# Kernel optimization log

Measured on AMD Instinct MI355X. Metric: run time of the kernel, lower is better.

Reference implementation:

```python
import jax, jax.numpy as jnp
import numpy as np

NUM_HEADS = 8
HEAD_SPLITS = [2, 3, 3]   # heads per conv window group (windows 3,5,7)


def _dwconv(x, w, b):
    # depthwise conv2d, SAME padding; x [B,Cg,H,W], w [Cg,1,k,k]
    k = w.shape[-1]
    pad = k // 2
    out = jax.lax.conv_general_dilated(
        x, w, window_strides=(1, 1), padding=[(pad, pad), (pad, pad)],
        feature_group_count=x.shape[1])
    return out + b[None, :, None, None]


def setup_inputs() -> dict:
    key = jax.random.key(0)
    ks = jax.random.split(key, 8)
    B, Hs, Ws, C = 16, 56, 56, 512
    N = 1 + Hs * Ws
    Ch = C // NUM_HEADS
    inp = {
        "x": jax.random.normal(ks[0], (B, N, C), dtype=jnp.float32),
        "qkv_w": jax.random.normal(ks[1], (3 * C, C), dtype=jnp.float32) * 0.02,
        "qkv_b": jnp.zeros((3 * C,), dtype=jnp.float32),
        "proj_w": jax.random.normal(ks[2], (C, C), dtype=jnp.float32) * 0.02,
        "proj_b": jnp.zeros((C,), dtype=jnp.float32),
        "conv_w3": jax.random.normal(ks[3], (2 * Ch, 1, 3, 3), dtype=jnp.float32) * 0.1,
        "conv_b3": jnp.zeros((2 * Ch,), dtype=jnp.float32),
        "conv_w5": jax.random.normal(ks[4], (3 * Ch, 1, 5, 5), dtype=jnp.float32) * 0.1,
        "conv_b5": jnp.zeros((3 * Ch,), dtype=jnp.float32),
        "conv_w7": jax.random.normal(ks[5], (3 * Ch, 1, 7, 7), dtype=jnp.float32) * 0.1,
        "conv_b7": jnp.zeros((3 * Ch,), dtype=jnp.float32),
        "H": 56,
        "W": 56,
    }
    return inp


def reference(x, qkv_w, qkv_b, proj_w, proj_b,
              conv_w3, conv_b3, conv_w5, conv_b5, conv_w7, conv_b7, H, W):
    B, N, C = x.shape
    h = NUM_HEADS
    Ch = C // h
    scale = Ch ** -0.5

    # qkv projection -> [3, B, h, N, Ch]
    qkv = (x @ qkv_w.T + qkv_b).reshape(B, N, 3, h, Ch)
    qkv = jnp.transpose(qkv, (2, 0, 3, 1, 4))
    q, k, v = qkv[0], qkv[1], qkv[2]

    # linear-attention factorization: softmax over tokens, then small Ch x Ch matmuls
    k_sm = jax.nn.softmax(k, axis=2)                     # softmax over N
    kv = jnp.einsum('bhnk,bhnd->bhkd', k_sm, v)          # [B,h,Ch,Ch]
    factor_att = jnp.einsum('bhnk,bhkd->bhnd', q, kv)    # [B,h,N,Ch]

    # conv relative-position encoding (CoaT ConvRelPosEnc)
    q_img = q[:, :, 1:, :]                               # drop CLS token
    v_img = v[:, :, 1:, :]
    v_img = jnp.transpose(v_img, (0, 1, 3, 2)).reshape(B, h * Ch, H, W)
    splits = np.cumsum([s * Ch for s in HEAD_SPLITS])[:-1]
    p3, p5, p7 = jnp.split(v_img, splits, axis=1)
    conv_v = jnp.concatenate([
        _dwconv(p3, conv_w3, conv_b3),
        _dwconv(p5, conv_w5, conv_b5),
        _dwconv(p7, conv_w7, conv_b7)], axis=1)           # [B,h*Ch,H,W]
    conv_v = jnp.transpose(conv_v.reshape(B, h, Ch, H * W), (0, 1, 3, 2))
    ev = q_img * conv_v                                   # [B,h,HW,Ch]
    crpe = jnp.concatenate(
        [jnp.zeros((B, h, 1, Ch), dtype=x.dtype), ev], axis=2)

    out = scale * factor_att + crpe                       # [B,h,N,Ch]
    out = jnp.transpose(out, (0, 2, 1, 3)).reshape(B, N, C)
    return out @ proj_w.T + proj_b
```

## Files before the change

kernel.cpp:

```cpp
#include <hip/hip_runtime.h>
#include <stdint.h>

#define NHEADS 8
#define NTOK   3137
#define BATCH  16
#define CDIM   512
#define MT     (BATCH*NTOK)

typedef unsigned short u16;
typedef float f32x4  __attribute__((ext_vector_type(4)));
typedef short bf16x8 __attribute__((ext_vector_type(8)));

__device__ __forceinline__ float bf2f(u16 u){
  union { uint32_t i; float f; } x; x.i = ((uint32_t)u) << 16; return x.f;
}
__device__ __forceinline__ u16 f2bf(float f){
  union { float f; uint32_t i; } x; x.f = f;
  uint32_t r = x.i + 0x7fffu + ((x.i >> 16) & 1u);
  return (u16)(r >> 16);
}
__device__ __forceinline__ void async_ld16(void* lds, const void* g){
  __builtin_amdgcn_global_load_lds((const __attribute__((address_space(1))) void*)g,
                                   (__attribute__((address_space(3))) void*)lds, 16, 0, 0);
}
#define BARM()   asm volatile("s_barrier" ::: "memory")
#define WAITV(N) asm volatile("s_waitcnt vmcnt(" #N ")" ::: "memory")
#define MFMA16(d,a,b) d = __builtin_amdgcn_mfma_f32_16x16x32_bf16(a,b,d,0,0,0)

__global__ void cvt_all(const float* __restrict__ x, u16* __restrict__ x_bf,
                        const float* __restrict__ qw, u16* __restrict__ qw_bf,
                        const float* __restrict__ pw, u16* __restrict__ pw_bf){
  const int n4x = (MT*512)/4, n4q = (1536*512)/4, n4p = (512*512)/4;
  int i = blockIdx.x * blockDim.x + threadIdx.x;
  const float* src; u16* dst; int j = i;
  if (i < n4x){ src = x; dst = x_bf; }
  else if (i < n4x + n4q){ src = qw; dst = qw_bf; j = i - n4x; }
  else if (i < n4x + n4q + n4p){ src = pw; dst = pw_bf; j = i - n4x - n4q; }
  else return;
  float4 v = ((const float4*)src)[j];
  uint32_t lo = ((uint32_t)f2bf(v.y) << 16) | f2bf(v.x);
  uint32_t hi = ((uint32_t)f2bf(v.w) << 16) | f2bf(v.z);
  ((uint2*)dst)[j] = make_uint2(lo, hi);
}

template<int MODE>
__global__ __launch_bounds__(256) void gemmM(
    const u16* __restrict__ A, const u16* __restrict__ Bw, const float* __restrict__ bias,
    u16* __restrict__ q_s, u16* __restrict__ k_s, u16* __restrict__ v_s,
    float* __restrict__ outF, int M)
{
  __shared__ __align__(16) u16 smem[256*64];
  const int t = threadIdx.x;
  const int w = t >> 6, l = t & 63;
  const int wr = w >> 1, wc = w & 1;
  const int lr = l & 15, lg = l >> 4;

  const int nx = gridDim.x;
  const int nwg = nx * gridDim.y;
  const int orig = blockIdx.y * nx + blockIdx.x;
  const int q8 = nwg >> 3, r8 = nwg & 7;
  const int xcd = orig & 7;
  const int wgid = (xcd < r8 ? xcd*(q8+1) : r8*(q8+1) + (xcd-r8)*q8) + (orig >> 3);
  const int n0 = (wgid % nx) * 128;
  const int m0 = (wgid / nx) * 128;

  f32x4 acc[4][4];
#pragma unroll
  for (int i=0;i<4;i++)
#pragma unroll
    for (int j=0;j<4;j++) acc[i][j] = (f32x4){0.f,0.f,0.f,0.f};

  u16* da = smem;
  u16* db = smem + 128*64;

  for (int kt = 0; kt < 8; ++kt){
    const int k0 = kt*64;
#pragma unroll
    for (int j=0;j<4;j++){
      int qc = t + 256*j;
      int R = qc >> 3, c = qc & 7;
      int cs = (c ^ (R & 7)) * 8;
      int ar = m0 + R; if (ar > M-1) ar = M-1;
      async_ld16(&da[qc*8], &A[(size_t)ar*512 + k0 + cs]);
    }
#pragma unroll
    for (int j=0;j<4;j++){
      int qc = t + 256*j;
      int R = qc >> 3, c = qc & 7;
      int cs = (c ^ (R & 7)) * 8;
      async_ld16(&db[qc*8], &Bw[(size_t)(n0+R)*512 + k0 + cs]);
    }
    WAITV(0);
    BARM();
    __builtin_amdgcn_s_setprio(1);
#pragma unroll
    for (int ks=0; ks<2; ks++){
      bf16x8 af[4], bfv[4];
      int chunk = ks*4 + lg;
#pragma unroll
      for (int fi=0;fi<4;fi++){
        int row = wr*64 + fi*16 + lr;
        af[fi] = *(const bf16x8*)&da[row*64 + ((chunk ^ (row & 7))*8)];
      }
#pragma unroll
      for (int fj=0;fj<4;fj++){
        int col = wc*64 + fj*16 + lr;
        bfv[fj] = *(const bf16x8*)&db[col*64 + ((chunk ^ (col & 7))*8)];
      }
#pragma unroll
      for (int fi=0;fi<4;fi++)
#pragma unroll
        for (int fj=0;fj<4;fj++)
          acc[fi][fj] = __builtin_amdgcn_mfma_f32_16x16x32_bf16(af[fi], bfv[fj], acc[fi][fj], 0, 0, 0);
    }
    __builtin_amdgcn_s_setprio(0);
    BARM();
  }

  float bvv[4];
#pragma unroll
  for (int fj=0;fj<4;fj++) bvv[fj] = bias[n0 + wc*64 + fj*16 + lr];
  const int colo = n0 + wc*64;

  if (MODE == 0){
    u16* warea = smem + w * 4096;
#pragma unroll
    for (int fi=0;fi<4;fi++)
#pragma unroll
      for (int fj=0;fj<4;fj++)
#pragma unroll
        for (int r=0;r<4;r++)
          warea[(fi*16 + lg*4 + r)*64 + fj*16 + lr] = f2bf(acc[fi][fj][r] + bvv[fj]);
    const int part = colo >> 9;
    const int hq   = (colo >> 6) & 7;
    u16* dst = (part == 0) ? q_s : ((part == 1) ? k_s : v_s);
    const int rsub = l >> 3;
    const int csub = (l & 7) * 8;
#pragma unroll
    for (int pass=0; pass<8; ++pass){
      int rl = pass*8 + rsub;
      int m = m0 + wr*64 + rl;
      if (m < M){
        int bb = m / NTOK;
        int n  = m - bb*NTOK;
        uint4 vv = *(const uint4*)&warea[rl*64 + csub];
        *(uint4*)&dst[((size_t)(bb*8 + hq)*NTOK + n)*64 + csub] = vv;
      }
    }
  } else {
    float* warea = (float*)smem + w * 2048;
    const int rsub = l >> 4;
    const int csub = (l & 15) * 4;
#pragma unroll
    for (int p=0; p<2; ++p){
#pragma unroll
      for (int fh=0; fh<2; fh++){
        int fi = p*2 + fh;
#pragma unroll
        for (int fj=0;fj<4;fj++)
#pragma unroll
          for (int r=0;r<4;r++)
            warea[(fh*16 + lg*4 + r)*64 + fj*16 + lr] = acc[fi][fj][r] + bvv[fj];
      }
#pragma unroll
      for (int pass=0; pass<8; ++pass){
        int rl = pass*4 + rsub;
        int m = m0 + wr*64 + p*32 + rl;
        if (m < M){
          float4 vv = *(const float4*)&warea[rl*64 + csub];
          *(float4*)&outF[(size_t)m*512 + colo + csub] = vv;
        }
      }
    }
  }
}

__global__ __launch_bounds__(256) void kv_mfma(
    const u16* __restrict__ k_s, const u16* __restrict__ v_s,
    float* __restrict__ kv_p, float* __restrict__ s_p)
{
  __shared__ __align__(16) u16 ekT[64*64];
  __shared__ __align__(16) u16 vT[64*64];
  __shared__ float part_s[32*64];
  const int t  = threadIdx.x;
  const int bh = blockIdx.x;
  const int qq = blockIdx.y;
  const size_t base = (size_t)bh * NTOK * 64;
  const int c_beg = qq*6 + (qq < 2 ? qq : 2);
  const int c_end = c_beg + 6 + (qq < 2 ? 1 : 0);
  const int w = t >> 6, l = t & 63;
  const int lr = l & 15, lg = l >> 4;
  const int nl0 = t >> 3;
  const int dc  = (t & 7) * 8;

  f32x4 acc[4];
#pragma unroll
  for (int j=0;j<4;j++) acc[j] = (f32x4){0.f,0.f,0.f,0.f};
  float s_loc[8];
#pragma unroll
  for (int i=0;i<8;i++) s_loc[i] = 0.f;

  auto LD = [&](int ch, int half, uint4& kv, uint4& vv){
    int n = ch*64 + nl0 + half*32;
    if (n < NTOK){
      kv = *(const uint4*)&k_s[base + (size_t)n*64 + dc];
      vv = *(const uint4*)&v_s[base + (size_t)n*64 + dc];
    } else {
      kv = make_uint4(0u,0u,0u,0u);
      vv = make_uint4(0u,0u,0u,0u);
    }
  };

  uint4 kc0, vc0, kc1, vc1, kn0, vn0, kn1, vn1;
  LD(c_beg, 0, kc0, vc0);
  LD(c_beg, 1, kc1, vc1);

  for (int ch = c_beg; ch < c_end; ++ch){
    const int n0c = ch*64;
    if (ch + 1 < c_end){ LD(ch+1, 0, kn0, vn0); LD(ch+1, 1, kn1, vn1); }
    __syncthreads();
#pragma unroll
    for (int half=0; half<2; ++half){
      const uint4& kvec = half ? kc1 : kc0;
      const uint4& vvec = half ? vc1 : vc0;
      int nloc = nl0 + half*32;
      bool valid = (n0c + nloc < NTOK);
      const u16* kp = (const u16*)&kvec;
      const u16* vp = (const u16*)&vvec;
      const int nc = nloc >> 3, ne = nloc & 7;
#pragma unroll
      for (int i=0;i<8;i++){
        float e = valid ? __expf(bf2f(kp[i])) : 0.f;
        s_loc[i] += e;
        int row = dc + i;
        int pos = row*64 + ((nc ^ (row & 7) ^ ((row >> 3) & 7))*8) + ne;
        ekT[pos] = f2bf(e);
        vT[pos]  = vp[i];
      }
    }
    __syncthreads();
    __builtin_amdgcn_s_setprio(1);
#pragma unroll
    for (int ks=0; ks<2; ks++){
      int chnk = ks*4 + lg;
      int arow = w*16 + lr;
      bf16x8 af = *(const bf16x8*)&ekT[arow*64 + ((chnk ^ (arow & 7) ^ ((arow >> 3) & 7))*8)];
#pragma unroll
      for (int fj=0; fj<4; fj++){
        int col = fj*16 + lr;
        bf16x8 bv = *(const bf16x8*)&vT[col*64 + ((chnk ^ (col & 7) ^ ((col >> 3) & 7))*8)];
        MFMA16(acc[fj], af, bv);
      }
    }
    __builtin_amdgcn_s_setprio(0);
    kc0 = kn0; vc0 = vn0; kc1 = kn1; vc1 = vn1;
  }

  const size_t obase = ((size_t)qq*128 + bh) * 4096;
#pragma unroll
  for (int fj=0; fj<4; fj++)
#pragma unroll
    for (int r=0; r<4; r++)
      kv_p[obase + (size_t)(w*16 + lg*4 + r)*64 + fj*16 + lr] = acc[fj][r];

#pragma unroll
  for (int i=0;i<8;i++) part_s[nl0*64 + dc + i] = s_loc[i];
  __syncthreads();
  if (t < 64){
    float s = 0.f;
    for (int r=0;r<32;r++) s += part_s[r*64 + t];
    s_p[((size_t)qq*128 + bh)*64 + t] = s;
  }
}

__global__ void kv_reduce(const float* __restrict__ kv_p, const float* __restrict__ s_p,
                          const u16* __restrict__ q_s, u16* __restrict__ kvT,
                          u16* __restrict__ out_pre){
  __shared__ float red[64*64];
  const int bh = blockIdx.x, t = threadIdx.x;
  const int b = bh >> 3, h = bh & 7;
  const int k = t >> 2;
  const float q0 = bf2f(q_s[(size_t)bh*NTOK*64 + k]);
  float S = 0.f;
#pragma unroll
  for (int hf=0; hf<8; hf++) S += s_p[(hf*128 + bh)*64 + k];
  const float rS = 1.f / S;
  for (int i=0;i<16;i++){
    int e = t*16 + i;
    int d = (t & 3)*16 + i;
    float v = 0.f;
#pragma unroll
    for (int hf=0; hf<8; hf++) v += kv_p[(size_t)(hf*128 + bh)*4096 + e];
    float val = v * rS;
    kvT[(size_t)bh*4096 + d*64 + k] = f2bf(val);
    red[k*64 + d] = val * q0;
  }
  __syncthreads();
  if (t < 64){
    float s = 0.f;
    for (int r=0;r<64;r++) s += red[r*64 + t];
    out_pre[((size_t)b*NTOK)*CDIM + h*64 + t] = f2bf(0.125f * s);
  }
}

template<int R>
__global__ __launch_bounds__(256) void conv_fa(
    const u16* __restrict__ v_s, const u16* __restrict__ q_s,
    const u16* __restrict__ kvT,
    const float* __restrict__ wsrc, const float* __restrict__ bsrc,
    int h0, u16* __restrict__ out_pre)
{
  constexpr int KK = 2*R + 1;
  constexpr int TAPS = KK*KK;
  __shared__ __align__(16) u16 smem[8192 + KK*3584];
  u16* vt = smem + 8192;
  const int t = threadIdx.x;
  const int y  = blockIdx.x;
  const int hh = blockIdx.y;
  const int b  = blockIdx.z;
  const int h  = h0 + hh;
  const int bh = b*8 + h;
  const size_t base = (size_t)bh * NTOK * 64;
  const int n0 = 1 + y*56;

#pragma unroll
  for (int j=0;j<2;j++){
    int qq = t + 256*j;
    int row = qq >> 3, c = qq & 7;
    int cs = (c ^ (row & 7)) * 8;
    int n = n0 + row; if (n > NTOK-1) n = NTOK-1;
    async_ld16(&smem[qq*8], &q_s[base + (size_t)n*64 + cs]);
    async_ld16(&smem[4096 + qq*8], &kvT[(size_t)bh*4096 + row*64 + cs]);
  }
  for (int ry=0; ry<KK; ry++){
    int yy = y - R + ry;
    for (int idx = t; idx < 448; idx += 256){
      uint4 val = make_uint4(0u,0u,0u,0u);
      if (yy >= 0 && yy < 56)
        val = *(const uint4*)&v_s[base + (size_t)(1 + yy*56)*64 + idx*8];
      *(uint4*)&vt[ry*3584 + idx*8] = val;
    }
  }
  __syncthreads();

  const int w = t >> 6, l = t & 63;
  const int lr = l & 15, lg = l >> 4;
  f32x4 fac[4];
#pragma unroll
  for (int j=0;j<4;j++) fac[j] = (f32x4){0.f,0.f,0.f,0.f};
#pragma unroll
  for (int ks=0; ks<2; ks++){
    int chunk = ks*4 + lg;
    int arow = w*16 + lr;
    bf16x8 af = *(const bf16x8*)&smem[arow*64 + ((chunk ^ (arow & 7))*8)];
#pragma unroll
    for (int fj=0; fj<4; fj++){
      int col = fj*16 + lr;
      bf16x8 bvv = *(const bf16x8*)&smem[4096 + col*64 + ((chunk ^ (col & 7))*8)];
      MFMA16(fac[fj], af, bvv);
    }
  }

  const int d = l;
  const int xg = w;
  float wreg[TAPS];
#pragma unroll
  for (int i=0;i<TAPS;i++) wreg[i] = wsrc[(hh*64 + d)*TAPS + i];
  const float bias = bsrc[hh*64 + d];
  float creg[14];
#pragma unroll
  for (int i=0;i<14;i++) creg[i] = bias;
  const int x0 = xg * 14;
#pragma unroll
  for (int ry=0; ry<KK; ry++){
    float rw[14 + 2*R];
#pragma unroll
    for (int i=0; i<14+2*R; i++){
      int xx = x0 - R + i;
      rw[i] = (xx >= 0 && xx < 56) ? bf2f(vt[ry*3584 + xx*64 + d]) : 0.f;
    }
#pragma unroll
    for (int xi=0; xi<14; xi++)
#pragma unroll
      for (int rx=0; rx<KK; rx++)
        creg[xi] += rw[xi+rx] * wreg[ry*KK + rx];
  }

  float qv[14];
#pragma unroll
  for (int xi=0; xi<14; xi++){
    int row = x0 + xi;
    int chunk = d >> 3, e = d & 7;
    qv[xi] = bf2f(smem[row*64 + ((chunk ^ (row & 7))*8) + e]);
  }

  __syncthreads();
  float* fa = (float*)smem;
#pragma unroll
  for (int fj=0; fj<4; fj++)
#pragma unroll
    for (int r=0; r<4; r++)
      fa[(w*16 + lg*4 + r)*64 + fj*16 + lr] = 0.125f * fac[fj][r];
  __syncthreads();

#pragma unroll
  for (int xi=0; xi<14; xi++){
    int nn = n0 + x0 + xi;
    out_pre[((size_t)b*NTOK + nn)*CDIM + h*64 + d] =
        f2bf(fa[(x0 + xi)*64 + d] + creg[xi]*qv[xi]);
  }
}

extern "C" void kernel_launch(void* const* d_in, const int* in_sizes, int n_in,
                              void* d_out, int out_size, void* d_ws, size_t ws_size,
                              hipStream_t stream)
{
  const float* x      = (const float*)d_in[0];
  const float* qkv_w  = (const float*)d_in[1];
  const float* qkv_b  = (const float*)d_in[2];
  const float* proj_w = (const float*)d_in[3];
  const float* proj_b = (const float*)d_in[4];
  const float* w3 = (const float*)d_in[5];
  const float* b3 = (const float*)d_in[6];
  const float* w5 = (const float*)d_in[7];
  const float* b5 = (const float*)d_in[8];
  const float* w7 = (const float*)d_in[9];
  const float* b7 = (const float*)d_in[10];
  float* out = (float*)d_out;

  char* ws = (char*)d_ws;
  size_t off = 0;
  auto alloc = [&](size_t bytes) -> void* {
    void* p = ws + off;
    off += (bytes + 255) & ~(size_t)255;
    return p;
  };
  u16*   x_bf     = (u16*)alloc((size_t)MT*512*2);
  u16*   qkvw_bf  = (u16*)alloc((size_t)1536*512*2);
  u16*   projw_bf = (u16*)alloc((size_t)512*512*2);
  u16*   q_s      = (u16*)alloc((size_t)128*NTOK*64*2);
  u16*   k_s      = (u16*)alloc((size_t)128*NTOK*64*2);
  u16*   v_s      = (u16*)alloc((size_t)128*NTOK*64*2);
  u16*   kvT      = (u16*)alloc((size_t)128*4096*2);
  float* kv_p     = (float*)alloc((size_t)8*128*4096*4);
  float* s_p      = (float*)alloc((size_t)8*128*64*4);
  u16*   out_pre  = x_bf;

  { int n4 = (MT*512 + 1536*512 + 512*512)/4;
    cvt_all<<<(n4+255)/256, 256, 0, stream>>>(x, x_bf, qkv_w, qkvw_bf, proj_w, projw_bf); }

  gemmM<0><<<dim3(12, 393), 256, 0, stream>>>(x_bf, qkvw_bf, qkv_b, q_s, k_s, v_s, nullptr, MT);

  kv_mfma<<<dim3(128, 8), 256, 0, stream>>>(k_s, v_s, kv_p, s_p);
  kv_reduce<<<128, 256, 0, stream>>>(kv_p, s_p, q_s, kvT, out_pre);

  conv_fa<1><<<dim3(56, 2, 16), 256, 0, stream>>>(v_s, q_s, kvT, w3, b3, 0, out_pre);
  conv_fa<2><<<dim3(56, 3, 16), 256, 0, stream>>>(v_s, q_s, kvT, w5, b5, 2, out_pre);
  conv_fa<3><<<dim3(56, 3, 16), 256, 0, stream>>>(v_s, q_s, kvT, w7, b7, 5, out_pre);

  gemmM<1><<<dim3(4, 393), 256, 0, stream>>>(out_pre, projw_bf, proj_b, nullptr, nullptr, nullptr, out, MT);
}
```

Measured before the change: 342.4 us.

## Use larger 256x256 tiled GEMM for projection and split kv_reduce across blocks

Adds a dedicated projection GEMM kernel with 256x256 tiles, 512 threads, and double-buffered async LDS loads, replacing the templated 128x128 path for the output projection. The larger tile raises arithmetic intensity per loaded tile and halves the number of workgroups. The kv_reduce kernel is also split over four d-quarters to increase parallelism and shrink its shared buffer. In exchange, the projection launches fewer workgroups (394) and has higher register and LDS pressure, which may limit occupancy.

```diff
diff --git a/kernel.cpp b/kernel.cpp
--- a/kernel.cpp
+++ b/kernel.cpp
@@ -43,11 +43,9 @@
   ((uint2*)dst)[j] = make_uint2(lo, hi);
 }
 
-template<int MODE>
 __global__ __launch_bounds__(256) void gemmM(
     const u16* __restrict__ A, const u16* __restrict__ Bw, const float* __restrict__ bias,
-    u16* __restrict__ q_s, u16* __restrict__ k_s, u16* __restrict__ v_s,
-    float* __restrict__ outF, int M)
+    u16* __restrict__ q_s, u16* __restrict__ k_s, u16* __restrict__ v_s, int M)
 {
   __shared__ __align__(16) u16 smem[256*64];
   const int t = threadIdx.x;
@@ -122,54 +120,142 @@
   for (int fj=0;fj<4;fj++) bvv[fj] = bias[n0 + wc*64 + fj*16 + lr];
   const int colo = n0 + wc*64;
 
-  if (MODE == 0){
-    u16* warea = smem + w * 4096;
-#pragma unroll
-    for (int fi=0;fi<4;fi++)
-#pragma unroll
-      for (int fj=0;fj<4;fj++)
+  u16* warea = smem + w * 4096;
+#pragma unroll
+  for (int fi=0;fi<4;fi++)
+#pragma unroll
+    for (int fj=0;fj<4;fj++)
+#pragma unroll
+      for (int r=0;r<4;r++)
+        warea[(fi*16 + lg*4 + r)*64 + fj*16 + lr] = f2bf(acc[fi][fj][r] + bvv[fj]);
+  const int part = colo >> 9;
+  const int hq   = (colo >> 6) & 7;
+  u16* dst = (part == 0) ? q_s : ((part == 1) ? k_s : v_s);
+  const int rsub = l >> 3;
+  const int csub = (l & 7) * 8;
+#pragma unroll
+  for (int pass=0; pass<8; ++pass){
+    int rl = pass*8 + rsub;
+    int m = m0 + wr*64 + rl;
+    if (m < M){
+      int bb = m / NTOK;
+      int n  = m - bb*NTOK;
+      uint4 vv = *(const uint4*)&warea[rl*64 + csub];
+      *(uint4*)&dst[((size_t)(bb*8 + hq)*NTOK + n)*64 + csub] = vv;
+    }
+  }
+}
+
+__global__ __launch_bounds__(512, 2) void gemmP(
+    const u16* __restrict__ A, const u16* __restrict__ Bw, const float* __restrict__ bias,
+    float* __restrict__ outF, int M)
+{
+  constexpr int BM=256, BN=256, WN=4;
+  constexpr int THREADS = 512;
+  constexpr int MF = 8, NF = 4;
+  constexpr int WROWS = 128, WCOLS = 64;
+  __shared__ __align__(16) u16 smem[2*(BM+BN)*64];
+
+  const int t = threadIdx.x;
+  const int w = t >> 6, l = t & 63;
+  const int wr = w / WN, wc = w % WN;
+  const int lr = l & 15, lg = l >> 4;
+
+  const int nx = gridDim.x;
+  const int nwg = nx * gridDim.y;
+  const int orig = blockIdx.y * nx + blockIdx.x;
+  const int q8 = nwg >> 3, r8 = nwg & 7;
+  const int xcd = orig & 7;
+  const int wgid = (xcd < r8 ? xcd*(q8+1) : r8*(q8+1) + (xcd-r8)*q8) + (orig >> 3);
+  const int n0 = (wgid % nx) * BN;
+  const int m0 = (wgid / nx) * BM;
+
+  f32x4 acc[MF][NF];
+#pragma unroll
+  for (int i=0;i<MF;i++)
+#pragma unroll
+    for (int j=0;j<NF;j++) acc[i][j] = (f32x4){0.f,0.f,0.f,0.f};
+
+  auto stage = [&](int bi, int k0){
+    u16* da = smem + bi*(BM*64);
+    u16* db = smem + 2*BM*64 + bi*(BN*64);
+#pragma unroll
+    for (int j=0;j<(BM*8)/THREADS;j++){
+      int qc = t + THREADS*j;
+      int R = qc >> 3, c = qc & 7;
+      int cs = (c ^ (R & 7)) * 8;
+      int ar = m0 + R; if (ar > M-1) ar = M-1;
+      async_ld16(&da[qc*8], &A[(size_t)ar*512 + k0 + cs]);
+    }
+#pragma unroll
+    for (int j=0;j<(BN*8)/THREADS;j++){
+      int qc = t + THREADS*j;
+      int R = qc >> 3, c = qc & 7;
+      int cs = (c ^ (R & 7)) * 8;
+      async_ld16(&db[qc*8], &Bw[(size_t)(n0+R)*512 + k0 + cs]);
+    }
+  };
+
+  stage(0, 0);
+  __syncthreads();
+  int cur = 0;
+  for (int kt = 0; kt < 8; ++kt){
+    if (kt < 7) stage(cur ^ 1, (kt+1)*64);
+    const u16* a_base = smem + cur*(BM*64);
+    const u16* b_base = smem + 2*BM*64 + cur*(BN*64);
+    __builtin_amdgcn_s_setprio(1);
+#pragma unroll
+    for (int ks=0; ks<2; ks++){
+      bf16x8 af[MF], bfv[NF];
+      int chunk = ks*4 + lg;
+#pragma unroll
+      for (int fi=0;fi<MF;fi++){
+        int row = wr*WROWS + fi*16 + lr;
+        af[fi] = *(const bf16x8*)&a_base[row*64 + ((chunk ^ (row & 7))*8)];
+      }
+#pragma unroll
+      for (int fj=0;fj<NF;fj++){
+        int col = wc*WCOLS + fj*16 + lr;
+        bfv[fj] = *(const bf16x8*)&b_base[col*64 + ((chunk ^ (col & 7))*8)];
+      }
+#pragma unroll
+      for (int fi=0;fi<MF;fi++)
+#pragma unroll
+        for (int fj=0;fj<NF;fj++)
+          acc[fi][fj] = __builtin_amdgcn_mfma_f32_16x16x32_bf16(af[fi], bfv[fj], acc[fi][fj], 0, 0, 0);
+    }
+    __builtin_amdgcn_s_setprio(0);
+    __syncthreads();
+    cur ^= 1;
+  }
+
+  float bvv[NF];
+#pragma unroll
+  for (int fj=0;fj<NF;fj++) bvv[fj] = bias[n0 + wc*WCOLS + fj*16 + lr];
+
+  constexpr int PR = WROWS/2;
+  float* warea = (float*)smem + w * (PR*WCOLS);
+  const int colo = n0 + wc*WCOLS;
+  const int rsub = l >> 4;
+  const int csub = (l & 15) * 4;
+#pragma unroll
+  for (int p=0; p<2; ++p){
+#pragma unroll
+    for (int fh=0; fh<MF/2; fh++){
+      int fi = p*(MF/2) + fh;
+#pragma unroll
+      for (int fj=0;fj<NF;fj++)
 #pragma unroll
         for (int r=0;r<4;r++)
-          warea[(fi*16 + lg*4 + r)*64 + fj*16 + lr] = f2bf(acc[fi][fj][r] + bvv[fj]);
-    const int part = colo >> 9;
-    const int hq   = (colo >> 6) & 7;
-    u16* dst = (part == 0) ? q_s : ((part == 1) ? k_s : v_s);
-    const int rsub = l >> 3;
-    const int csub = (l & 7) * 8;
-#pragma unroll
-    for (int pass=0; pass<8; ++pass){
-      int rl = pass*8 + rsub;
-      int m = m0 + wr*64 + rl;
+          warea[(fh*16 + lg*4 + r)*WCOLS + fj*16 + lr] = acc[fi][fj][r] + bvv[fj];
+    }
+#pragma unroll
+    for (int pass=0; pass<PR/4; ++pass){
+      int rl = pass*4 + rsub;
+      int m = m0 + wr*WROWS + p*PR + rl;
       if (m < M){
-        int bb = m / NTOK;
-        int n  = m - bb*NTOK;
-        uint4 vv = *(const uint4*)&warea[rl*64 + csub];
-        *(uint4*)&dst[((size_t)(bb*8 + hq)*NTOK + n)*64 + csub] = vv;
-      }
-    }
-  } else {
-    float* warea = (float*)smem + w * 2048;
-    const int rsub = l >> 4;
-    const int csub = (l & 15) * 4;
-#pragma unroll
-    for (int p=0; p<2; ++p){
-#pragma unroll
-      for (int fh=0; fh<2; fh++){
-        int fi = p*2 + fh;
-#pragma unroll
-        for (int fj=0;fj<4;fj++)
-#pragma unroll
-          for (int r=0;r<4;r++)
-            warea[(fh*16 + lg*4 + r)*64 + fj*16 + lr] = acc[fi][fj][r] + bvv[fj];
-      }
-#pragma unroll
-      for (int pass=0; pass<8; ++pass){
-        int rl = pass*4 + rsub;
-        int m = m0 + wr*64 + p*32 + rl;
-        if (m < M){
-          float4 vv = *(const float4*)&warea[rl*64 + csub];
-          *(float4*)&outF[(size_t)m*512 + colo + csub] = vv;
-        }
+        float4 vv = *(const float4*)&warea[rl*WCOLS + csub];
+        *(float4*)&outF[(size_t)m*512 + colo + csub] = vv;
       }
     }
   }
@@ -276,8 +362,8 @@
 __global__ void kv_reduce(const float* __restrict__ kv_p, const float* __restrict__ s_p,
                           const u16* __restrict__ q_s, u16* __restrict__ kvT,
                           u16* __restrict__ out_pre){
-  __shared__ float red[64*64];
-  const int bh = blockIdx.x, t = threadIdx.x;
+  __shared__ float red[64*16];
+  const int bh = blockIdx.x, dq = blockIdx.y, t = threadIdx.x;
   const int b = bh >> 3, h = bh & 7;
   const int k = t >> 2;
   const float q0 = bf2f(q_s[(size_t)bh*NTOK*64 + k]);
@@ -285,21 +371,23 @@
 #pragma unroll
   for (int hf=0; hf<8; hf++) S += s_p[(hf*128 + bh)*64 + k];
   const float rS = 1.f / S;
-  for (int i=0;i<16;i++){
-    int e = t*16 + i;
-    int d = (t & 3)*16 + i;
+#pragma unroll
+  for (int i=0;i<4;i++){
+    int dsub = (t & 3)*4 + i;
+    int d = dq*16 + dsub;
+    int e = k*64 + d;
     float v = 0.f;
 #pragma unroll
     for (int hf=0; hf<8; hf++) v += kv_p[(size_t)(hf*128 + bh)*4096 + e];
     float val = v * rS;
     kvT[(size_t)bh*4096 + d*64 + k] = f2bf(val);
-    red[k*64 + d] = val * q0;
+    red[k*16 + dsub] = val * q0;
   }
   __syncthreads();
-  if (t < 64){
+  if (t < 16){
     float s = 0.f;
-    for (int r=0;r<64;r++) s += red[r*64 + t];
-    out_pre[((size_t)b*NTOK)*CDIM + h*64 + t] = f2bf(0.125f * s);
+    for (int r=0;r<64;r++) s += red[r*16 + t];
+    out_pre[((size_t)b*NTOK)*CDIM + h*64 + dq*16 + t] = f2bf(0.125f * s);
   }
 }
 
@@ -449,14 +537,14 @@
   { int n4 = (MT*512 + 1536*512 + 512*512)/4;
     cvt_all<<<(n4+255)/256, 256, 0, stream>>>(x, x_bf, qkv_w, qkvw_bf, proj_w, projw_bf); }
 
-  gemmM<0><<<dim3(12, 393), 256, 0, stream>>>(x_bf, qkvw_bf, qkv_b, q_s, k_s, v_s, nullptr, MT);
+  gemmM<<<dim3(12, 393), 256, 0, stream>>>(x_bf, qkvw_bf, qkv_b, q_s, k_s, v_s, MT);
 
   kv_mfma<<<dim3(128, 8), 256, 0, stream>>>(k_s, v_s, kv_p, s_p);
-  kv_reduce<<<128, 256, 0, stream>>>(kv_p, s_p, q_s, kvT, out_pre);
+  kv_reduce<<<dim3(128, 4), 256, 0, stream>>>(kv_p, s_p, q_s, kvT, out_pre);
 
   conv_fa<1><<<dim3(56, 2, 16), 256, 0, stream>>>(v_s, q_s, kvT, w3, b3, 0, out_pre);
   conv_fa<2><<<dim3(56, 3, 16), 256, 0, stream>>>(v_s, q_s, kvT, w5, b5, 2, out_pre);
   conv_fa<3><<<dim3(56, 3, 16), 256, 0, stream>>>(v_s, q_s, kvT, w7, b7, 5, out_pre);
 
-  gemmM<1><<<dim3(4, 393), 256, 0, stream>>>(out_pre, projw_bf, proj_b, nullptr, nullptr, nullptr, out, MT);
-}
+  gemmP<<<dim3(2, 197), 512, 0, stream>>>(out_pre, projw_bf, proj_b, out, MT);
+}
```

New measurement: 340.5 us. Within noise of the previous version (-0.5%).
